# Optimization experiments

Measured on AMD Instinct MI355X. Metric: run time of the kernel, lower is better.

## Reference

```python
import jax, jax.numpy as jnp
import numpy as np

WS = 8          # window_size
NH = 8          # num_heads
DIM = 256
INNER = 256     # inner_dim (QK)
CINNER = 64     # coords_inner_dim
INNER_V = 256


def _rms(x, g, eps=1e-6):
    return x * jax.lax.rsqrt(jnp.mean(x * x, axis=-1, keepdims=True) + eps) * g


def _window(x, ws):
    # (b, H, W, d) -> (b, Wh, Ww, ws*ws, d)
    b, H, W, d = x.shape
    Wh, Ww = H // ws, W // ws
    x = x.reshape(b, Wh, ws, Ww, ws, d).transpose(0, 1, 3, 2, 4, 5)
    return x.reshape(b, Wh, Ww, ws * ws, d)


def _unwindow(x, Wh, Ww, ws):
    # (b, Wh*Ww, ws*ws, d) -> (b, Wh*ws, Ww*ws, d)
    b = x.shape[0]
    d = x.shape[-1]
    x = x.reshape(b, Wh, Ww, ws, ws, d).transpose(0, 1, 3, 2, 4, 5)
    return x.reshape(b, Wh * ws, Ww * ws, d)


def _embed_source(x, c, fqk_w, fqk_b, fqk_g, cqk_w, cqk_b, cqk_g, v_w):
    b = x.shape[0]
    xw = _window(x, WS)           # (b, Wh, Ww, n, dim)
    cw = _window(c, WS)
    Wh, Ww = xw.shape[1], xw.shape[2]
    f_avg = xw.mean(axis=3)       # (b, Wh, Ww, dim)
    c_avg = cw.mean(axis=3)
    f_qk = _rms(f_avg @ fqk_w.T + fqk_b, fqk_g).reshape(b, Wh * Ww, 2 * INNER)
    c_qk = _rms(c_avg @ cqk_w.T + cqk_b, cqk_g).reshape(b, Wh * Ww, 2 * CINNER)
    v = (xw @ v_w.T).reshape(b, Wh * Ww, WS * WS * INNER_V)
    return f_qk, c_qk, v, (Wh, Ww)


def setup_inputs() -> dict:
    key = jax.random.key(0)
    ks = jax.random.split(key, 8)
    s = 0.02
    return {
        "x1": jax.random.normal(ks[0], (4, 128, 128, DIM), jnp.float32),
        "c1": jax.random.normal(ks[1], (4, 128, 128, 4), jnp.float32),
        "x2": jax.random.normal(ks[2], (4, 96, 96, DIM), jnp.float32),
        "c2": jax.random.normal(ks[3], (4, 96, 96, 4), jnp.float32),
        "fqk_w": jax.random.normal(ks[4], (2 * INNER, DIM), jnp.float32) * s,
        "fqk_b": jnp.zeros((2 * INNER,), jnp.float32),
        "fqk_g": jnp.ones((2 * INNER,), jnp.float32),
        "cqk_w": jax.random.normal(ks[5], (2 * CINNER, 4), jnp.float32) * s,
        "cqk_b": jnp.zeros((2 * CINNER,), jnp.float32),
        "cqk_g": jnp.ones((2 * CINNER,), jnp.float32),
        "v_w": jax.random.normal(ks[6], (INNER_V, DIM), jnp.float32) * s,
        "vb_w": jax.random.normal(ks[7], (DIM, INNER_V), jnp.float32) * s,
    }


def reference(x1, c1, x2, c2, fqk_w, fqk_b, fqk_g, cqk_w, cqk_b, cqk_g, v_w, vb_w):
    b = x1.shape[0]
    f1, cc1, v1, (Wh1, Ww1) = _embed_source(x1, c1, fqk_w, fqk_b, fqk_g, cqk_w, cqk_b, cqk_g, v_w)
    f2, cc2, v2, (Wh2, Ww2) = _embed_source(x2, c2, fqk_w, fqk_b, fqk_g, cqk_w, cqk_b, cqk_g, v_w)
    n1, n2 = Wh1 * Ww1, Wh2 * Ww2
    N = n1 + n2

    f_qk = jnp.concatenate([f1, f2], axis=1)   # (b, N, 2*INNER)
    c_qk = jnp.concatenate([cc1, cc2], axis=1) # (b, N, 2*CINNER)
    values = jnp.concatenate([v1, v2], axis=1) # (b, N, WS*WS*INNER_V)

    f_q, f_k = jnp.split(f_qk, 2, axis=-1)
    c_q, c_k = jnp.split(c_qk, 2, axis=-1)

    dh = INNER // NH
    dch = CINNER // NH
    dv = values.shape[-1] // NH
    fq = f_q.reshape(b, N, NH, dh)
    fk = f_k.reshape(b, N, NH, dh)
    cq = c_q.reshape(b, N, NH, dch)
    ck = c_k.reshape(b, N, NH, dch)
    vh = values.reshape(b, N, NH, dv)

    scores = jnp.einsum("bnhd,bmhd->bhnm", fq, fk) / np.sqrt(dh)
    scores = scores + jnp.einsum("bnhd,bmhd->bhnm", cq, ck) / np.sqrt(dch)

    # mask self-attention within each source (block-diagonal masked out)
    seg = jnp.concatenate([jnp.zeros((n1,), jnp.int32), jnp.ones((n2,), jnp.int32)])
    allowed = seg[:, None] != seg[None, :]                     # (N, N) True = keep
    scores = jnp.where(allowed[None, None], scores, jnp.finfo(scores.dtype).min)

    attn = jax.nn.softmax(scores, axis=-1)                      # (b, h, N, N)
    v_out = jnp.einsum("bhnm,bmhd->bnhd", attn, vh).reshape(b, N, NH * dv)

    v_out = v_out.reshape(b, N, WS * WS, INNER_V)
    features_out = v_out @ vb_w.T                               # (b, N, ws*ws, dim)

    out1 = _unwindow(features_out[:, :n1], Wh1, Ww1, WS)
    out2 = _unwindow(features_out[:, n1:], Wh2, Ww2, WS)
    return out1, out2
```

## Files before the change

kernel.cpp:

```cpp
#include <hip/hip_runtime.h>
#include <hip/hip_bf16.h>

#define B 4
#define NH 8
#define N1 256
#define N2 144
#define NW 400
#define OUT2_OFF ((size_t)16777216)

typedef __attribute__((ext_vector_type(8))) short short8v;
typedef __attribute__((ext_vector_type(4))) float f32x4;
typedef __attribute__((ext_vector_type(2))) unsigned uint2v;
typedef __attribute__((ext_vector_type(4))) unsigned uint4v;

static __device__ __forceinline__ short f2bf(float f) {
    __hip_bfloat16 h = __float2bfloat16(f);
    return __builtin_bit_cast(short, h);
}

static __device__ __forceinline__ const float* xrow_ptr(const float* x1, const float* x2,
                                                        int b, int n, int p) {
    if (n < N1)
        return x1 + (((size_t)b * 128 + (n >> 4) * 8 + (p >> 3)) * 128 + (n & 15) * 8 + (p & 7)) * 256;
    int nn = n - N1;
    return x2 + (((size_t)b * 96 + (nn / 12) * 8 + (p >> 3)) * 96 + (nn % 12) * 8 + (p & 7)) * 256;
}

__global__ void prep_kernel(const float* __restrict__ v_w, const float* __restrict__ vb_w,
                            short* __restrict__ Mbf) {
    int d = blockIdx.x;
    int k = threadIdx.x;
    float s = 0.f;
    for (int j = 0; j < 256; ++j)
        s += vb_w[d * 256 + j] * v_w[j * 256 + k];
    size_t idx = ((((size_t)((d >> 4) * 8 + (k >> 5))) * 4 + ((k >> 3) & 3)) * 16 + (d & 15)) * 8 + (k & 7);
    Mbf[idx] = f2bf(s);
}

__global__ void wconv_kernel(const float* __restrict__ fqk_w, short* __restrict__ fqk_wb) {
    int i = blockIdx.x * 256 + threadIdx.x;
    fqk_wb[i] = f2bf(fqk_w[i]);
}

__global__ void mean_kernel(const float* __restrict__ x1, const float* __restrict__ c1,
                            const float* __restrict__ x2, const float* __restrict__ c2,
                            const float* __restrict__ cqk_w, const float* __restrict__ cqk_b,
                            const float* __restrict__ cqk_g,
                            short* __restrict__ favgb,
                            short* __restrict__ qcat, short* __restrict__ kcat) {
    int blk = blockIdx.x;
    int b = blk / NW, n = blk % NW;
    int t = threadIdx.x;

    __shared__ float cavg[4];
    __shared__ float red[256];

    const float* xbase;
    int rstride;
    if (n < N1) {
        xbase = x1 + (((size_t)b * 128 + (n >> 4) * 8) * 128 + (n & 15) * 8) * 256;
        rstride = 128 * 256;
    } else {
        int nn = n - N1;
        xbase = x2 + (((size_t)b * 96 + (nn / 12) * 8) * 96 + (nn % 12) * 8) * 256;
        rstride = 96 * 256;
    }

    float a0 = 0.f, a1 = 0.f, a2 = 0.f, a3 = 0.f;
    #pragma unroll
    for (int pr = 0; pr < 8; ++pr) {
        const float* rowp = xbase + (size_t)pr * rstride + t;
        a0 += rowp[0 * 256] + rowp[4 * 256];
        a1 += rowp[1 * 256] + rowp[5 * 256];
        a2 += rowp[2 * 256] + rowp[6 * 256];
        a3 += rowp[3 * 256] + rowp[7 * 256];
    }
    favgb[(size_t)blk * 256 + t] = f2bf((a0 + a1 + a2 + a3) * (1.f / 64.f));

    if (t < 64) {
        const float* cbase;
        int crs;
        if (n < N1) {
            cbase = c1 + (((size_t)b * 128 + (n >> 4) * 8) * 128 + (n & 15) * 8) * 4;
            crs = 128 * 4;
        } else {
            int nn = n - N1;
            cbase = c2 + (((size_t)b * 96 + (nn / 12) * 8) * 96 + (nn % 12) * 8) * 4;
            crs = 96 * 4;
        }
        float4 v = *(const float4*)(cbase + (t >> 3) * crs + (t & 7) * 4);
        for (int off = 32; off > 0; off >>= 1) {
            v.x += __shfl_down(v.x, off, 64);
            v.y += __shfl_down(v.y, off, 64);
            v.z += __shfl_down(v.z, off, 64);
            v.w += __shfl_down(v.w, off, 64);
        }
        if (t == 0) {
            cavg[0] = v.x * (1.f / 64.f);
            cavg[1] = v.y * (1.f / 64.f);
            cavg[2] = v.z * (1.f / 64.f);
            cavg[3] = v.w * (1.f / 64.f);
        }
    }
    __syncthreads();

    float co = 0.f;
    if (t < 128) {
        co = cqk_b[t];
        #pragma unroll
        for (int k = 0; k < 4; ++k) co += cavg[k] * cqk_w[t * 4 + k];
    }
    red[t] = (t < 128) ? co * co : 0.f;
    __syncthreads();
    for (int s = 128; s > 0; s >>= 1) {
        if (t < s) red[t] += red[t + s];
        __syncthreads();
    }
    float cscale = rsqrtf(red[0] / 128.f + 1e-6f);

    const float SC = 0.35355339059327373f;
    if (t < 64) {
        int h = t >> 3, j = 32 + (t & 7);
        qcat[((size_t)(b * 8 + h) * NW + n) * 64 + j] = f2bf(co * cscale * cqk_g[t] * SC);
    } else if (t < 128) {
        int tt = t - 64;
        int h = tt >> 3, j = 32 + (tt & 7);
        kcat[((size_t)(b * 8 + h) * NW + n) * 64 + j] = f2bf(co * cscale * cqk_g[t]);
    } else {
        int tt = t - 128;
        for (int z = tt; z < 384; z += 128) {
            int which = z & 1;
            int zz = z >> 1;
            int h = zz / 24, j = 40 + zz % 24;
            short* dst = which ? kcat : qcat;
            dst[((size_t)(b * 8 + h) * NW + n) * 64 + j] = 0;
        }
    }
}

__global__ __launch_bounds__(256) void qkproj_kernel(const short* __restrict__ fqk_wb,
                                                     const float* __restrict__ fqk_b,
                                                     const float* __restrict__ fqk_g,
                                                     const short* __restrict__ favgb,
                                                     short* __restrict__ qcat,
                                                     short* __restrict__ kcat) {
    int w = threadIdx.x >> 6, lane = threadIdx.x & 63;
    int ngl = w >> 1, half = w & 1;
    int ngrp = blockIdx.x * 2 + ngl;
    int l15 = lane & 15, g = lane >> 4;

    __shared__ float ssb[2][2][16];

    const short* frow = favgb + ((size_t)ngrp * 16 + l15) * 256;
    short8v bf[8];
    #pragma unroll
    for (int c = 0; c < 8; ++c) bf[c] = *(const short8v*)(frow + c * 32 + g * 8);

    f32x4 acc[16];
    #pragma unroll
    for (int i = 0; i < 16; ++i) acc[i] = (f32x4)0.f;

    #pragma unroll
    for (int mt = 0; mt < 16; ++mt) {
        const short* arow = fqk_wb + ((size_t)(half * 256 + mt * 16 + l15)) * 256;
        #pragma unroll
        for (int c = 0; c < 8; ++c) {
            short8v af = *(const short8v*)(arow + c * 32 + g * 8);
            acc[mt] = __builtin_amdgcn_mfma_f32_16x16x32_bf16(af, bf[c], acc[mt], 0, 0, 0);
        }
    }

    float ss = 0.f;
    #pragma unroll
    for (int mt = 0; mt < 16; ++mt) {
        float4 bi = *(const float4*)(fqk_b + half * 256 + mt * 16 + g * 4);
        acc[mt][0] += bi.x; acc[mt][1] += bi.y; acc[mt][2] += bi.z; acc[mt][3] += bi.w;
        ss += acc[mt][0] * acc[mt][0] + acc[mt][1] * acc[mt][1]
            + acc[mt][2] * acc[mt][2] + acc[mt][3] * acc[mt][3];
    }
    ss += __shfl_xor(ss, 16, 64);
    ss += __shfl_xor(ss, 32, 64);
    if (lane < 16) ssb[ngl][half][lane] = ss;
    __syncthreads();
    float scale = rsqrtf((ssb[ngl][0][l15] + ssb[ngl][1][l15]) / 512.f + 1e-6f);

    int idx = ngrp * 16 + l15;
    int b = idx / NW, n = idx % NW;
    const float SF = 0.17677669529663687f;
    float mult = half ? 1.f : SF;
    short* dst = half ? kcat : qcat;

    #pragma unroll
    for (int mt = 0; mt < 16; ++mt) {
        int ol = mt * 16 + g * 4;
        float4 gg = *(const float4*)(fqk_g + half * 256 + ol);
        int h = ol >> 5, j = ol & 31;
        short4 s4 = make_short4(f2bf(acc[mt][0] * scale * gg.x * mult),
                                f2bf(acc[mt][1] * scale * gg.y * mult),
                                f2bf(acc[mt][2] * scale * gg.z * mult),
                                f2bf(acc[mt][3] * scale * gg.w * mult));
        *(short4*)(dst + ((size_t)(b * 8 + h) * NW + n) * 64 + j) = s4;
    }
}

template <int NMT>
static __device__ __forceinline__ void scores_wave(const short* __restrict__ qcat,
                                                   const short* __restrict__ kcat,
                                                   short* __restrict__ Pb,
                                                   int b, int h, int n0, int mbase, int lane) {
    int l15 = lane & 15, g = lane >> 4;
    int kl8 = g * 8;
    size_t rowb = (size_t)(b * 8 + h) * NW;

    const short* qrow = qcat + (rowb + n0 + l15) * 64;
    short8v bf0 = *(const short8v*)(qrow + kl8);
    short8v bf1 = *(const short8v*)(qrow + 32 + kl8);

    f32x4 acc[NMT];
    #pragma unroll
    for (int i = 0; i < NMT; ++i) acc[i] = (f32x4)0.f;

    #pragma unroll
    for (int mt = 0; mt < NMT; ++mt) {
        const short* krow = kcat + (rowb + mbase + mt * 16 + l15) * 64;
        short8v af0 = *(const short8v*)(krow + kl8);
        short8v af1 = *(const short8v*)(krow + 32 + kl8);
        acc[mt] = __builtin_amdgcn_mfma_f32_16x16x32_bf16(af0, bf0, acc[mt], 0, 0, 0);
        acc[mt] = __builtin_amdgcn_mfma_f32_16x16x32_bf16(af1, bf1, acc[mt], 0, 0, 0);
    }

    float mx = -3.4e38f;
    #pragma unroll
    for (int mt = 0; mt < NMT; ++mt)
        #pragma unroll
        for (int r = 0; r < 4; ++r) mx = fmaxf(mx, acc[mt][r]);
    mx = fmaxf(mx, __shfl_xor(mx, 16, 64));
    mx = fmaxf(mx, __shfl_xor(mx, 32, 64));

    float sum = 0.f;
    #pragma unroll
    for (int mt = 0; mt < NMT; ++mt)
        #pragma unroll
        for (int r = 0; r < 4; ++r) {
            float e = __expf(acc[mt][r] - mx);
            acc[mt][r] = e;
            sum += e;
        }
    sum += __shfl_xor(sum, 16, 64);
    sum += __shfl_xor(sum, 32, 64);
    float inv = 1.f / sum;

    int n = n0 + l15;
    short* prow = Pb + ((size_t)(b * 8 + h) * 512 + n) * 416;
    #pragma unroll
    for (int mt = 0; mt < NMT; ++mt) {
        int m = mbase + mt * 16 + g * 4;
        *(short4*)(prow + m) = make_short4(f2bf(acc[mt][0] * inv), f2bf(acc[mt][1] * inv),
                                           f2bf(acc[mt][2] * inv), f2bf(acc[mt][3] * inv));
    }
}

__global__ __launch_bounds__(256) void scores_kernel(const short* __restrict__ qcat,
                                                     const short* __restrict__ kcat,
                                                     short* __restrict__ Pb) {
    int wid = blockIdx.x * 4 + (threadIdx.x >> 6);
    int lane = threadIdx.x & 63;
    if (wid < 512) {
        int b = wid >> 7, h = (wid >> 4) & 7, n0 = (wid & 15) * 16;
        scores_wave<9>(qcat, kcat, Pb, b, h, n0, 256, lane);
    } else {
        int t3 = wid - 512;
        int b = t3 / 72, r = t3 % 72;
        int h = r / 9, n0 = 256 + (r % 9) * 16;
        scores_wave<16>(qcat, kcat, Pb, b, h, n0, 0, lane);
    }
}

__global__ __launch_bounds__(256, 2) void wproj_mfma(const float* __restrict__ x1,
                                                     const float* __restrict__ x2,
                                                     const short* __restrict__ Mbf,
                                                     short* __restrict__ Wb) {
    int bid = blockIdx.x;
    int dt = bid & 1, rh = (bid >> 1) & 1, rt = bid >> 2;
    int tid = threadIdx.x;
    int lane = tid & 63, w = tid >> 6;
    int wd = w & 1, wrR = w >> 1;
    int l15 = lane & 15, g = lane >> 4;

    __shared__ short lds[2][128][40];

    int b = rt / 100;
    int nb0 = (rt % 100) * 4 + rh * 2;

    int Rl0 = tid >> 2, oc = tid & 3;
    int Rl1 = Rl0 + 64;
    const float* src0 = xrow_ptr(x1, x2, b, nb0 + (Rl0 >> 6), Rl0 & 63) + oc * 8;
    const float* src1 = xrow_ptr(x1, x2, b, nb0 + (Rl1 >> 6), Rl1 & 63) + oc * 8;

    float4 p00 = *(const float4*)(src0);
    float4 p01 = *(const float4*)(src0 + 4);
    float4 p10 = *(const float4*)(src1);
    float4 p11 = *(const float4*)(src1 + 4);

    f32x4 acc[4][4] = {};
    for (int kc = 0; kc < 8; ++kc) {
        int buf = kc & 1;
        short8v s0, s1;
        s0[0] = f2bf(p00.x); s0[1] = f2bf(p00.y); s0[2] = f2bf(p00.z); s0[3] = f2bf(p00.w);
        s0[4] = f2bf(p01.x); s0[5] = f2bf(p01.y); s0[6] = f2bf(p01.z); s0[7] = f2bf(p01.w);
        s1[0] = f2bf(p10.x); s1[1] = f2bf(p10.y); s1[2] = f2bf(p10.z); s1[3] = f2bf(p10.w);
        s1[4] = f2bf(p11.x); s1[5] = f2bf(p11.y); s1[6] = f2bf(p11.z); s1[7] = f2bf(p11.w);
        *(short8v*)&lds[buf][Rl0][oc * 8] = s0;
        *(short8v*)&lds[buf][Rl1][oc * 8] = s1;
        if (kc < 7) {
            const float* q0 = src0 + (kc + 1) * 32;
            const float* q1 = src1 + (kc + 1) * 32;
            p00 = *(const float4*)q0; p01 = *(const float4*)(q0 + 4);
            p10 = *(const float4*)q1; p11 = *(const float4*)(q1 + 4);
        }
        short8v af[4];
        #pragma unroll
        for (int mi = 0; mi < 4; ++mi) {
            int dtile = dt * 8 + wd * 4 + mi;
            af[mi] = *(const short8v*)(Mbf + ((size_t)(dtile * 8 + kc)) * 512 + lane * 8);
        }
        __syncthreads();
        #pragma unroll
        for (int ni = 0; ni < 4; ++ni) {
            int Rl = wrR * 64 + ni * 16 + l15;
            short8v bfv = *(const short8v*)&lds[buf][Rl][g * 8];
            #pragma unroll
            for (int mi = 0; mi < 4; ++mi)
                acc[mi][ni] = __builtin_amdgcn_mfma_f32_16x16x32_bf16(af[mi], bfv, acc[mi][ni], 0, 0, 0);
        }
    }

    int dq = dt * 128 + wd * 64 + g * 4;
    #pragma unroll
    for (int ni = 0; ni < 4; ++ni) {
        size_t Rg = (size_t)rt * 256 + rh * 128 + wrR * 64 + ni * 16 + l15;
        short* wp = Wb + Rg * 256 + dq;
        #pragma unroll
        for (int mi = 0; mi < 4; ++mi) {
            f32x4 a = acc[mi][ni];
            *(short4*)(wp + mi * 16) = make_short4(f2bf(a[0]), f2bf(a[1]), f2bf(a[2]), f2bf(a[3]));
        }
    }
}

__global__ __launch_bounds__(256, 2) void pv_mfma(
    const short* __restrict__ Pb, const short* __restrict__ Wb,
    float* __restrict__ out) {
    int bid = blockIdx.x;
    int dt = bid & 1;
    int nt = (bid >> 1) & 3;
    int p  = (bid >> 3) & 63;
    int b  = bid >> 9;
    int h  = p >> 3;
    int tid = threadIdx.x;
    int lane = tid & 63;
    int w = tid >> 6;
    int wr = w >> 1;
    int wc = w & 1;
    int l15 = lane & 15;
    int kl8 = (lane >> 4) << 3;

    __shared__ short8v Bs[512];
    unsigned ldsBase = (unsigned)(size_t)&Bs[0];

    int n0 = nt * 128;
    int mlo = (nt < 2) ? 256 : 0;
    int mhi = (nt < 2) ? 400 : 256;
    int d0 = dt * 128;

    const short* arow[4];
    #pragma unroll
    for (int mi = 0; mi < 4; ++mi) {
        int n = n0 + wr * 64 + mi * 16 + l15;
        arow[mi] = Pb + ((size_t)(b * 8 + h) * 512 + n) * 416 + kl8;
    }

    f32x4 acc[4][4] = {};

    int mrow0 = tid >> 4;
    int doff0 = (tid & 15) << 3;
    int mrow1 = (tid + 256) >> 4;
    int doff1 = doff0;

    const size_t wbBase = ((size_t)b * 400) * 64 * 256 + (size_t)p * 256 + d0;

    short8v cur0, cur1;
    {
        int gm0 = mlo + mrow0, gm1 = mlo + mrow1;
        cur0 = (gm0 < mhi) ? *(const short8v*)(Wb + wbBase + (size_t)gm0 * 64 * 256 + doff0) : (short8v)0;
        cur1 = (gm1 < mhi) ? *(const short8v*)(Wb + wbBase + (size_t)gm1 * 64 * 256 + doff1) : (short8v)0;
    }

    for (int m0 = mlo; m0 < mhi; m0 += 32) {
        short8v af[4];
        #pragma unroll
        for (int mi = 0; mi < 4; ++mi)
            af[mi] = *(const short8v*)(arow[mi] + m0);

        __syncthreads();
        {
            int par = (mrow0 >> 2) & 1, gg = mrow0 >> 3, r = mrow0 & 3;
            int nb = doff0 >> 4, c0h = (doff0 >> 3) & 1;
            Bs[(par * 8 + nb) * 32 + gg * 8 + r * 2 + c0h] = cur0;
            par = (mrow1 >> 2) & 1; gg = mrow1 >> 3; r = mrow1 & 3;
            nb = doff1 >> 4; c0h = (doff1 >> 3) & 1;
            Bs[(par * 8 + nb) * 32 + gg * 8 + r * 2 + c0h] = cur1;
        }
        if (m0 + 32 < mhi) {
            int gm0 = m0 + 32 + mrow0, gm1 = m0 + 32 + mrow1;
            cur0 = (gm0 < mhi) ? *(const short8v*)(Wb + wbBase + (size_t)gm0 * 64 * 256 + doff0) : (short8v)0;
            cur1 = (gm1 < mhi) ? *(const short8v*)(Wb + wbBase + (size_t)gm1 * 64 * 256 + doff1) : (short8v)0;
        }
        __syncthreads();

        short8v bfv[4];
        #pragma unroll
        for (int ni = 0; ni < 4; ++ni) {
            int nb = wc * 4 + ni;
            unsigned a0 = ldsBase + (unsigned)((0 * 8 + nb) * 512 + lane * 8);
            unsigned a1 = ldsBase + (unsigned)((1 * 8 + nb) * 512 + lane * 8);
            uint2v lo, hi;
            asm volatile("ds_read_b64_tr_b16 %0, %1" : "=v"(lo) : "v"(a0));
            asm volatile("ds_read_b64_tr_b16 %0, %1" : "=v"(hi) : "v"(a1));
            uint4v bw; bw.x = lo.x; bw.y = lo.y; bw.z = hi.x; bw.w = hi.y;
            bfv[ni] = __builtin_bit_cast(short8v, bw);
        }
        asm volatile("s_waitcnt lgkmcnt(0)" ::: "memory");
        __builtin_amdgcn_sched_barrier(0);

        #pragma unroll
        for (int mi = 0; mi < 4; ++mi) {
            #pragma unroll
            for (int ni = 0; ni < 4; ++ni)
                acc[mi][ni] = __builtin_amdgcn_mfma_f32_16x16x32_bf16(af[mi], bfv[ni], acc[mi][ni], 0, 0, 0);
        }
    }

    int pr = p >> 3, pc = p & 7;
    #pragma unroll
    for (int mi = 0; mi < 4; ++mi) {
        #pragma unroll
        for (int r = 0; r < 4; ++r) {
            int n = n0 + wr * 64 + mi * 16 + ((lane >> 4) << 2) + r;
            if (n >= NW) continue;
            float* obase;
            if (n < N1) {
                obase = out + (((size_t)b * 128 + (n >> 4) * 8 + pr) * 128 + ((n & 15) << 3) + pc) * 256;
            } else {
                int nn = n - N1;
                obase = out + OUT2_OFF + (((size_t)b * 96 + (nn / 12) * 8 + pr) * 96 + (nn % 12) * 8 + pc) * 256;
            }
            #pragma unroll
            for (int ni = 0; ni < 4; ++ni)
                obase[d0 + wc * 64 + ni * 16 + l15] = acc[mi][ni][r];
        }
    }
}

extern "C" void kernel_launch(void* const* d_in, const int* in_sizes, int n_in,
                              void* d_out, int out_size, void* d_ws, size_t ws_size,
                              hipStream_t stream) {
    const float* x1    = (const float*)d_in[0];
    const float* c1    = (const float*)d_in[1];
    const float* x2    = (const float*)d_in[2];
    const float* c2    = (const float*)d_in[3];
    const float* fqk_w = (const float*)d_in[4];
    const float* fqk_b = (const float*)d_in[5];
    const float* fqk_g = (const float*)d_in[6];
    const float* cqk_w = (const float*)d_in[7];
    const float* cqk_b = (const float*)d_in[8];
    const float* cqk_g = (const float*)d_in[9];
    const float* v_w   = (const float*)d_in[10];
    const float* vb_w  = (const float*)d_in[11];
    float* out = (float*)d_out;

    char* wsb = (char*)d_ws;
    short* Mbf    = (short*)(wsb);
    short* fqk_wb = (short*)(wsb + 131072);
    short* favgb  = (short*)(wsb + 393216);
    short* qcat   = (short*)(wsb + 1212416);
    short* kcat   = (short*)(wsb + 2850816);
    short* Pb     = (short*)(wsb + 4489216);
    short* Wb     = (short*)(wsb + 18120704);

    prep_kernel<<<256, 256, 0, stream>>>(v_w, vb_w, Mbf);
    wconv_kernel<<<512, 256, 0, stream>>>(fqk_w, fqk_wb);
    mean_kernel<<<B * NW, 256, 0, stream>>>(x1, c1, x2, c2, cqk_w, cqk_b, cqk_g,
                                            favgb, qcat, kcat);
    qkproj_kernel<<<50, 256, 0, stream>>>(fqk_wb, fqk_b, fqk_g, favgb, qcat, kcat);
    wproj_mfma<<<1600, 256, 0, stream>>>(x1, x2, Mbf, Wb);
    scores_kernel<<<200, 256, 0, stream>>>(qcat, kcat, Pb);
    pv_mfma<<<2048, 256, 0, stream>>>(Pb, Wb, out);
}
```

Measured before the change: 343.2 us.

## Merge setup and projection launches and enlarge pv_mfma blocks to 512 threads

Folds the prep, weight-convert and mean kernels into one setup_kernel dispatched by block index, and merges the qk projection into the W projection kernel, cutting the launch count from seven to four. pv_mfma now runs 512-thread blocks, each covering 256 query rows per half with one staged load per thread instead of two, halving the grid. The goal is to cut launch and tail gaps and reuse each staged W tile across more rows. In exchange, blocks in the merged kernels have uneven work, and the larger pv block changes occupancy and per-block sync cost.

```diff
diff --git a/kernel.cpp b/kernel.cpp
--- a/kernel.cpp
+++ b/kernel.cpp
@@ -26,34 +26,38 @@
     return x2 + (((size_t)b * 96 + (nn / 12) * 8 + (p >> 3)) * 96 + (nn % 12) * 8 + (p & 7)) * 256;
 }
 
-__global__ void prep_kernel(const float* __restrict__ v_w, const float* __restrict__ vb_w,
-                            short* __restrict__ Mbf) {
-    int d = blockIdx.x;
-    int k = threadIdx.x;
-    float s = 0.f;
-    for (int j = 0; j < 256; ++j)
-        s += vb_w[d * 256 + j] * v_w[j * 256 + k];
-    size_t idx = ((((size_t)((d >> 4) * 8 + (k >> 5))) * 4 + ((k >> 3) & 3)) * 16 + (d & 15)) * 8 + (k & 7);
-    Mbf[idx] = f2bf(s);
-}
-
-__global__ void wconv_kernel(const float* __restrict__ fqk_w, short* __restrict__ fqk_wb) {
-    int i = blockIdx.x * 256 + threadIdx.x;
-    fqk_wb[i] = f2bf(fqk_w[i]);
-}
-
-__global__ void mean_kernel(const float* __restrict__ x1, const float* __restrict__ c1,
-                            const float* __restrict__ x2, const float* __restrict__ c2,
-                            const float* __restrict__ cqk_w, const float* __restrict__ cqk_b,
-                            const float* __restrict__ cqk_g,
-                            short* __restrict__ favgb,
-                            short* __restrict__ qcat, short* __restrict__ kcat) {
-    int blk = blockIdx.x;
-    int b = blk / NW, n = blk % NW;
+__global__ void setup_kernel(const float* __restrict__ v_w, const float* __restrict__ vb_w,
+                             const float* __restrict__ fqk_w,
+                             const float* __restrict__ x1, const float* __restrict__ c1,
+                             const float* __restrict__ x2, const float* __restrict__ c2,
+                             const float* __restrict__ cqk_w, const float* __restrict__ cqk_b,
+                             const float* __restrict__ cqk_g,
+                             short* __restrict__ Mbf, short* __restrict__ fqk_wb,
+                             short* __restrict__ favgb,
+                             short* __restrict__ qcat, short* __restrict__ kcat) {
+    int bid = blockIdx.x;
     int t = threadIdx.x;
 
     __shared__ float cavg[4];
     __shared__ float red[256];
+
+    if (bid < 256) {
+        int d = bid, k = t;
+        float s = 0.f;
+        for (int j = 0; j < 256; ++j)
+            s += vb_w[d * 256 + j] * v_w[j * 256 + k];
+        size_t idx = ((((size_t)((d >> 4) * 8 + (k >> 5))) * 4 + ((k >> 3) & 3)) * 16 + (d & 15)) * 8 + (k & 7);
+        Mbf[idx] = f2bf(s);
+        return;
+    }
+    if (bid < 768) {
+        int i = (bid - 256) * 256 + t;
+        fqk_wb[i] = f2bf(fqk_w[i]);
+        return;
+    }
+
+    int blk = bid - 768;
+    int b = blk / NW, n = blk % NW;
 
     const float* xbase;
     int rstride;
@@ -138,156 +142,79 @@
     }
 }
 
-__global__ __launch_bounds__(256) void qkproj_kernel(const short* __restrict__ fqk_wb,
-                                                     const float* __restrict__ fqk_b,
-                                                     const float* __restrict__ fqk_g,
-                                                     const short* __restrict__ favgb,
-                                                     short* __restrict__ qcat,
-                                                     short* __restrict__ kcat) {
-    int w = threadIdx.x >> 6, lane = threadIdx.x & 63;
-    int ngl = w >> 1, half = w & 1;
-    int ngrp = blockIdx.x * 2 + ngl;
-    int l15 = lane & 15, g = lane >> 4;
-
+__global__ __launch_bounds__(256, 2) void projw_kernel(
+    const short* __restrict__ fqk_wb, const float* __restrict__ fqk_b,
+    const float* __restrict__ fqk_g, const short* __restrict__ favgb,
+    short* __restrict__ qcat, short* __restrict__ kcat,
+    const float* __restrict__ x1, const float* __restrict__ x2,
+    const short* __restrict__ Mbf, short* __restrict__ Wb) {
+    __shared__ short lds[2][128][40];
     __shared__ float ssb[2][2][16];
 
-    const short* frow = favgb + ((size_t)ngrp * 16 + l15) * 256;
-    short8v bf[8];
-    #pragma unroll
-    for (int c = 0; c < 8; ++c) bf[c] = *(const short8v*)(frow + c * 32 + g * 8);
-
-    f32x4 acc[16];
-    #pragma unroll
-    for (int i = 0; i < 16; ++i) acc[i] = (f32x4)0.f;
-
-    #pragma unroll
-    for (int mt = 0; mt < 16; ++mt) {
-        const short* arow = fqk_wb + ((size_t)(half * 256 + mt * 16 + l15)) * 256;
-        #pragma unroll
-        for (int c = 0; c < 8; ++c) {
-            short8v af = *(const short8v*)(arow + c * 32 + g * 8);
-            acc[mt] = __builtin_amdgcn_mfma_f32_16x16x32_bf16(af, bf[c], acc[mt], 0, 0, 0);
-        }
-    }
-
-    float ss = 0.f;
-    #pragma unroll
-    for (int mt = 0; mt < 16; ++mt) {
-        float4 bi = *(const float4*)(fqk_b + half * 256 + mt * 16 + g * 4);
-        acc[mt][0] += bi.x; acc[mt][1] += bi.y; acc[mt][2] += bi.z; acc[mt][3] += bi.w;
-        ss += acc[mt][0] * acc[mt][0] + acc[mt][1] * acc[mt][1]
-            + acc[mt][2] * acc[mt][2] + acc[mt][3] * acc[mt][3];
-    }
-    ss += __shfl_xor(ss, 16, 64);
-    ss += __shfl_xor(ss, 32, 64);
-    if (lane < 16) ssb[ngl][half][lane] = ss;
-    __syncthreads();
-    float scale = rsqrtf((ssb[ngl][0][l15] + ssb[ngl][1][l15]) / 512.f + 1e-6f);
-
-    int idx = ngrp * 16 + l15;
-    int b = idx / NW, n = idx % NW;
-    const float SF = 0.17677669529663687f;
-    float mult = half ? 1.f : SF;
-    short* dst = half ? kcat : qcat;
-
-    #pragma unroll
-    for (int mt = 0; mt < 16; ++mt) {
-        int ol = mt * 16 + g * 4;
-        float4 gg = *(const float4*)(fqk_g + half * 256 + ol);
-        int h = ol >> 5, j = ol & 31;
-        short4 s4 = make_short4(f2bf(acc[mt][0] * scale * gg.x * mult),
-                                f2bf(acc[mt][1] * scale * gg.y * mult),
-                                f2bf(acc[mt][2] * scale * gg.z * mult),
-                                f2bf(acc[mt][3] * scale * gg.w * mult));
-        *(short4*)(dst + ((size_t)(b * 8 + h) * NW + n) * 64 + j) = s4;
-    }
-}
-
-template <int NMT>
-static __device__ __forceinline__ void scores_wave(const short* __restrict__ qcat,
-                                                   const short* __restrict__ kcat,
-                                                   short* __restrict__ Pb,
-                                                   int b, int h, int n0, int mbase, int lane) {
-    int l15 = lane & 15, g = lane >> 4;
-    int kl8 = g * 8;
-    size_t rowb = (size_t)(b * 8 + h) * NW;
-
-    const short* qrow = qcat + (rowb + n0 + l15) * 64;
-    short8v bf0 = *(const short8v*)(qrow + kl8);
-    short8v bf1 = *(const short8v*)(qrow + 32 + kl8);
-
-    f32x4 acc[NMT];
-    #pragma unroll
-    for (int i = 0; i < NMT; ++i) acc[i] = (f32x4)0.f;
-
-    #pragma unroll
-    for (int mt = 0; mt < NMT; ++mt) {
-        const short* krow = kcat + (rowb + mbase + mt * 16 + l15) * 64;
-        short8v af0 = *(const short8v*)(krow + kl8);
-        short8v af1 = *(const short8v*)(krow + 32 + kl8);
-        acc[mt] = __builtin_amdgcn_mfma_f32_16x16x32_bf16(af0, bf0, acc[mt], 0, 0, 0);
-        acc[mt] = __builtin_amdgcn_mfma_f32_16x16x32_bf16(af1, bf1, acc[mt], 0, 0, 0);
-    }
-
-    float mx = -3.4e38f;
-    #pragma unroll
-    for (int mt = 0; mt < NMT; ++mt)
-        #pragma unroll
-        for (int r = 0; r < 4; ++r) mx = fmaxf(mx, acc[mt][r]);
-    mx = fmaxf(mx, __shfl_xor(mx, 16, 64));
-    mx = fmaxf(mx, __shfl_xor(mx, 32, 64));
-
-    float sum = 0.f;
-    #pragma unroll
-    for (int mt = 0; mt < NMT; ++mt)
-        #pragma unroll
-        for (int r = 0; r < 4; ++r) {
-            float e = __expf(acc[mt][r] - mx);
-            acc[mt][r] = e;
-            sum += e;
-        }
-    sum += __shfl_xor(sum, 16, 64);
-    sum += __shfl_xor(sum, 32, 64);
-    float inv = 1.f / sum;
-
-    int n = n0 + l15;
-    short* prow = Pb + ((size_t)(b * 8 + h) * 512 + n) * 416;
-    #pragma unroll
-    for (int mt = 0; mt < NMT; ++mt) {
-        int m = mbase + mt * 16 + g * 4;
-        *(short4*)(prow + m) = make_short4(f2bf(acc[mt][0] * inv), f2bf(acc[mt][1] * inv),
-                                           f2bf(acc[mt][2] * inv), f2bf(acc[mt][3] * inv));
-    }
-}
-
-__global__ __launch_bounds__(256) void scores_kernel(const short* __restrict__ qcat,
-                                                     const short* __restrict__ kcat,
-                                                     short* __restrict__ Pb) {
-    int wid = blockIdx.x * 4 + (threadIdx.x >> 6);
-    int lane = threadIdx.x & 63;
-    if (wid < 512) {
-        int b = wid >> 7, h = (wid >> 4) & 7, n0 = (wid & 15) * 16;
-        scores_wave<9>(qcat, kcat, Pb, b, h, n0, 256, lane);
-    } else {
-        int t3 = wid - 512;
-        int b = t3 / 72, r = t3 % 72;
-        int h = r / 9, n0 = 256 + (r % 9) * 16;
-        scores_wave<16>(qcat, kcat, Pb, b, h, n0, 0, lane);
-    }
-}
-
-__global__ __launch_bounds__(256, 2) void wproj_mfma(const float* __restrict__ x1,
-                                                     const float* __restrict__ x2,
-                                                     const short* __restrict__ Mbf,
-                                                     short* __restrict__ Wb) {
-    int bid = blockIdx.x;
-    int dt = bid & 1, rh = (bid >> 1) & 1, rt = bid >> 2;
     int tid = threadIdx.x;
     int lane = tid & 63, w = tid >> 6;
+    int l15 = lane & 15, g = lane >> 4;
+
+    if (blockIdx.x < 50) {
+        int ngl = w >> 1, half = w & 1;
+        int ngrp = blockIdx.x * 2 + ngl;
+
+        const short* frow = favgb + ((size_t)ngrp * 16 + l15) * 256;
+        short8v bf[8];
+        #pragma unroll
+        for (int c = 0; c < 8; ++c) bf[c] = *(const short8v*)(frow + c * 32 + g * 8);
+
+        f32x4 acc[16];
+        #pragma unroll
+        for (int i = 0; i < 16; ++i) acc[i] = (f32x4)0.f;
+
+        #pragma unroll
+        for (int mt = 0; mt < 16; ++mt) {
+            const short* arow = fqk_wb + ((size_t)(half * 256 + mt * 16 + l15)) * 256;
+            #pragma unroll
+            for (int c = 0; c < 8; ++c) {
+                short8v af = *(const short8v*)(arow + c * 32 + g * 8);
+                acc[mt] = __builtin_amdgcn_mfma_f32_16x16x32_bf16(af, bf[c], acc[mt], 0, 0, 0);
+            }
+        }
+
+        float ss = 0.f;
+        #pragma unroll
+        for (int mt = 0; mt < 16; ++mt) {
+            float4 bi = *(const float4*)(fqk_b + half * 256 + mt * 16 + g * 4);
+            acc[mt][0] += bi.x; acc[mt][1] += bi.y; acc[mt][2] += bi.z; acc[mt][3] += bi.w;
+            ss += acc[mt][0] * acc[mt][0] + acc[mt][1] * acc[mt][1]
+                + acc[mt][2] * acc[mt][2] + acc[mt][3] * acc[mt][3];
+        }
+        ss += __shfl_xor(ss, 16, 64);
+        ss += __shfl_xor(ss, 32, 64);
+        if (lane < 16) ssb[ngl][half][lane] = ss;
+        __syncthreads();
+        float scale = rsqrtf((ssb[ngl][0][l15] + ssb[ngl][1][l15]) / 512.f + 1e-6f);
+
+        int idx = ngrp * 16 + l15;
+        int b = idx / NW, n = idx % NW;
+        const float SF = 0.17677669529663687f;
+        float mult = half ? 1.f : SF;
+        short* dst = half ? kcat : qcat;
+
+        #pragma unroll
+        for (int mt = 0; mt < 16; ++mt) {
+            int ol = mt * 16 + g * 4;
+            float4 gg = *(const float4*)(fqk_g + half * 256 + ol);
+            int h = ol >> 5, j = ol & 31;
+            short4 s4 = make_short4(f2bf(acc[mt][0] * scale * gg.x * mult),
+                                    f2bf(acc[mt][1] * scale * gg.y * mult),
+                                    f2bf(acc[mt][2] * scale * gg.z * mult),
+                                    f2bf(acc[mt][3] * scale * gg.w * mult));
+            *(short4*)(dst + ((size_t)(b * 8 + h) * NW + n) * 64 + j) = s4;
+        }
+        return;
+    }
+
+    int bid = blockIdx.x - 50;
+    int dt = bid & 1, rh = (bid >> 1) & 1, rt = bid >> 2;
     int wd = w & 1, wrR = w >> 1;
-    int l15 = lane & 15, g = lane >> 4;
-
-    __shared__ short lds[2][128][40];
 
     int b = rt / 100;
     int nb0 = (rt % 100) * 4 + rh * 2;
@@ -348,15 +275,88 @@
     }
 }
 
-__global__ __launch_bounds__(256, 2) void pv_mfma(
+template <int NMT>
+static __device__ __forceinline__ void scores_wave(const short* __restrict__ qcat,
+                                                   const short* __restrict__ kcat,
+                                                   short* __restrict__ Pb,
+                                                   int b, int h, int n0, int mbase, int lane) {
+    int l15 = lane & 15, g = lane >> 4;
+    int kl8 = g * 8;
+    size_t rowb = (size_t)(b * 8 + h) * NW;
+
+    const short* qrow = qcat + (rowb + n0 + l15) * 64;
+    short8v bf0 = *(const short8v*)(qrow + kl8);
+    short8v bf1 = *(const short8v*)(qrow + 32 + kl8);
+
+    f32x4 acc[NMT];
+    #pragma unroll
+    for (int i = 0; i < NMT; ++i) acc[i] = (f32x4)0.f;
+
+    #pragma unroll
+    for (int mt = 0; mt < NMT; ++mt) {
+        const short* krow = kcat + (rowb + mbase + mt * 16 + l15) * 64;
+        short8v af0 = *(const short8v*)(krow + kl8);
+        short8v af1 = *(const short8v*)(krow + 32 + kl8);
+        acc[mt] = __builtin_amdgcn_mfma_f32_16x16x32_bf16(af0, bf0, acc[mt], 0, 0, 0);
+        acc[mt] = __builtin_amdgcn_mfma_f32_16x16x32_bf16(af1, bf1, acc[mt], 0, 0, 0);
+    }
+
+    float mx = -3.4e38f;
+    #pragma unroll
+    for (int mt = 0; mt < NMT; ++mt)
+        #pragma unroll
+        for (int r = 0; r < 4; ++r) mx = fmaxf(mx, acc[mt][r]);
+    mx = fmaxf(mx, __shfl_xor(mx, 16, 64));
+    mx = fmaxf(mx, __shfl_xor(mx, 32, 64));
+
+    float sum = 0.f;
+    #pragma unroll
+    for (int mt = 0; mt < NMT; ++mt)
+        #pragma unroll
+        for (int r = 0; r < 4; ++r) {
+            float e = __expf(acc[mt][r] - mx);
+            acc[mt][r] = e;
+            sum += e;
+        }
+    sum += __shfl_xor(sum, 16, 64);
+    sum += __shfl_xor(sum, 32, 64);
+    float inv = 1.f / sum;
+
+    int n = n0 + l15;
+    short* prow = Pb + ((size_t)(b * 8 + h) * 512 + n) * 416;
+    #pragma unroll
+    for (int mt = 0; mt < NMT; ++mt) {
+        int m = mbase + mt * 16 + g * 4;
+        *(short4*)(prow + m) = make_short4(f2bf(acc[mt][0] * inv), f2bf(acc[mt][1] * inv),
+                                           f2bf(acc[mt][2] * inv), f2bf(acc[mt][3] * inv));
+    }
+}
+
+__global__ __launch_bounds__(256) void scores_kernel(const short* __restrict__ qcat,
+                                                     const short* __restrict__ kcat,
+                                                     short* __restrict__ Pb) {
+    int wid = blockIdx.x * 4 + (threadIdx.x >> 6);
+    int lane = threadIdx.x & 63;
+    if (wid < 512) {
+        int b = wid >> 7, h = (wid >> 4) & 7, n0 = (wid & 15) * 16;
+        scores_wave<9>(qcat, kcat, Pb, b, h, n0, 256, lane);
+    } else {
+        int t3 = wid - 512;
+        int b = t3 / 72, r = t3 % 72;
+        int h = r / 9, n0 = 256 + (r % 9) * 16;
+        scores_wave<16>(qcat, kcat, Pb, b, h, n0, 0, lane);
+    }
+}
+
+__global__ __launch_bounds__(512) void pv_mfma(
     const short* __restrict__ Pb, const short* __restrict__ Wb,
     float* __restrict__ out) {
     int bid = blockIdx.x;
-    int dt = bid & 1;
-    int nt = (bid >> 1) & 3;
-    int p  = (bid >> 3) & 63;
-    int b  = bid >> 9;
-    int h  = p >> 3;
+    int dt   = bid & 1;
+    int half = (bid >> 1) & 1;
+    int p    = (bid >> 2) & 63;
+    int b    = bid >> 8;
+    int h    = p >> 3;
     int tid = threadIdx.x;
     int lane = tid & 63;
     int w = tid >> 6;
@@ -368,9 +368,9 @@
     __shared__ short8v Bs[512];
     unsigned ldsBase = (unsigned)(size_t)&Bs[0];
 
-    int n0 = nt * 128;
-    int mlo = (nt < 2) ? 256 : 0;
-    int mhi = (nt < 2) ? 400 : 256;
+    int n0 = half * 256;
+    int mlo = half ? 0 : 256;
+    int mhi = half ? 256 : 400;
     int d0 = dt * 128;
 
     const short* arow[4];
@@ -384,16 +384,16 @@
 
     int mrow0 = tid >> 4;
     int doff0 = (tid & 15) << 3;
-    int mrow1 = (tid + 256) >> 4;
-    int doff1 = doff0;
+    int par = (mrow0 >> 2) & 1, gg = mrow0 >> 3, r = mrow0 & 3;
+    int nb = doff0 >> 4, c0h = (doff0 >> 3) & 1;
+    int bsIdx = (par * 8 + nb) * 32 + gg * 8 + r * 2 + c0h;
 
     const size_t wbBase = ((size_t)b * 400) * 64 * 256 + (size_t)p * 256 + d0;
 
-    short8v cur0, cur1;
+    short8v cur0;
     {
-        int gm0 = mlo + mrow0, gm1 = mlo + mrow1;
+        int gm0 = mlo + mrow0;
         cur0 = (gm0 < mhi) ? *(const short8v*)(Wb + wbBase + (size_t)gm0 * 64 * 256 + doff0) : (short8v)0;
-        cur1 = (gm1 < mhi) ? *(const short8v*)(Wb + wbBase + (size_t)gm1 * 64 * 256 + doff1) : (short8v)0;
     }
 
     for (int m0 = mlo; m0 < mhi; m0 += 32) {
@@ -403,27 +403,19 @@
             af[mi] = *(const short8v*)(arow[mi] + m0);
 
         __syncthreads();
-        {
-            int par = (mrow0 >> 2) & 1, gg = mrow0 >> 3, r = mrow0 & 3;
-            int nb = doff0 >> 4, c0h = (doff0 >> 3) & 1;
-            Bs[(par * 8 + nb) * 32 + gg * 8 + r * 2 + c0h] = cur0;
-            par = (mrow1 >> 2) & 1; gg = mrow1 >> 3; r = mrow1 & 3;
-            nb = doff1 >> 4; c0h = (doff1 >> 3) & 1;
-            Bs[(par * 8 + nb) * 32 + gg * 8 + r * 2 + c0h] = cur1;
-        }
+        Bs[bsIdx] = cur0;
         if (m0 + 32 < mhi) {
-            int gm0 = m0 + 32 + mrow0, gm1 = m0 + 32 + mrow1;
+            int gm0 = m0 + 32 + mrow0;
             cur0 = (gm0 < mhi) ? *(const short8v*)(Wb + wbBase + (size_t)gm0 * 64 * 256 + doff0) : (short8v)0;
-            cur1 = (gm1 < mhi) ? *(const short8v*)(Wb + wbBase + (size_t)gm1 * 64 * 256 + doff1) : (short8v)0;
         }
         __syncthreads();
 
         short8v bfv[4];
         #pragma unroll
         for (int ni = 0; ni < 4; ++ni) {
-            int nb = wc * 4 + ni;
-            unsigned a0 = ldsBase + (unsigned)((0 * 8 + nb) * 512 + lane * 8);
-            unsigned a1 = ldsBase + (unsigned)((1 * 8 + nb) * 512 + lane * 8);
+            int nbr = wc * 4 + ni;
+            unsigned a0 = ldsBase + (unsigned)((0 * 8 + nbr) * 512 + lane * 8);
+            unsigned a1 = ldsBase + (unsigned)((1 * 8 + nbr) * 512 + lane * 8);
             uint2v lo, hi;
             asm volatile("ds_read_b64_tr_b16 %0, %1" : "=v"(lo) : "v"(a0));
             asm volatile("ds_read_b64_tr_b16 %0, %1" : "=v"(hi) : "v"(a1));
@@ -445,8 +437,8 @@
     #pragma unroll
     for (int mi = 0; mi < 4; ++mi) {
         #pragma unroll
-        for (int r = 0; r < 4; ++r) {
-            int n = n0 + wr * 64 + mi * 16 + ((lane >> 4) << 2) + r;
+        for (int rr = 0; rr < 4; ++rr) {
+            int n = n0 + wr * 64 + mi * 16 + ((lane >> 4) << 2) + rr;
             if (n >= NW) continue;
             float* obase;
             if (n < N1) {
@@ -457,7 +449,7 @@
             }
             #pragma unroll
             for (int ni = 0; ni < 4; ++ni)
-                obase[d0 + wc * 64 + ni * 16 + l15] = acc[mi][ni][r];
+                obase[d0 + wc * 64 + ni * 16 + l15] = acc[mi][ni][rr];
         }
     }
 }
@@ -488,12 +480,11 @@
     short* Pb     = (short*)(wsb + 4489216);
     short* Wb     = (short*)(wsb + 18120704);
 
-    prep_kernel<<<256, 256, 0, stream>>>(v_w, vb_w, Mbf);
-    wconv_kernel<<<512, 256, 0, stream>>>(fqk_w, fqk_wb);
-    mean_kernel<<<B * NW, 256, 0, stream>>>(x1, c1, x2, c2, cqk_w, cqk_b, cqk_g,
-                                            favgb, qcat, kcat);
-    qkproj_kernel<<<50, 256, 0, stream>>>(fqk_wb, fqk_b, fqk_g, favgb, qcat, kcat);
-    wproj_mfma<<<1600, 256, 0, stream>>>(x1, x2, Mbf, Wb);
+    setup_kernel<<<2368, 256, 0, stream>>>(v_w, vb_w, fqk_w, x1, c1, x2, c2,
+                                           cqk_w, cqk_b, cqk_g,
+                                           Mbf, fqk_wb, favgb, qcat, kcat);
+    projw_kernel<<<1650, 256, 0, stream>>>(fqk_wb, fqk_b, fqk_g, favgb, qcat, kcat,
+                                           x1, x2, Mbf, Wb);
     scores_kernel<<<200, 256, 0, stream>>>(qcat, kcat, Pb);
-    pv_mfma<<<2048, 256, 0, stream>>>(Pb, Wb, out);
-}
+    pv_mfma<<<1024, 512, 0, stream>>>(Pb, Wb, out);
+}
```

Result: faster. 311.6 us (-9.2%).
